# Performance work log

Measured on AMD Instinct MI355X. Metric: run time of the kernel, lower is better.

The kernel has to match this reference:

```python
import jax, jax.numpy as jnp
import numpy as np
import math

B, S, D, H = 2, 2048, 2048, 16
HD = D // H  # head_dim = 128


def _rope_tables(seq_len, head_dim, theta=10000.0):
    inv = 1.0 / (theta ** (np.arange(0, head_dim, 2, dtype=np.float32) / head_dim))
    t = np.arange(seq_len, dtype=np.float32)
    freqs = np.outer(t, inv)  # [S, HD/2]
    return jnp.asarray(np.cos(freqs)), jnp.asarray(np.sin(freqs))


def setup_inputs() -> dict:
    key = jax.random.key(0)
    ks = jax.random.split(key, 6)
    std = 1.0 / math.sqrt(D)
    x = jax.random.normal(ks[0], (B, S, D), dtype=jnp.float32)
    wq_w = jax.random.normal(ks[1], (D, D), dtype=jnp.float32) * std
    wk_w = jax.random.normal(ks[2], (D, D), dtype=jnp.float32) * std
    wv_w = jax.random.normal(ks[3], (D, D), dtype=jnp.float32) * std
    wo_w = jax.random.normal(ks[4], (D, D), dtype=jnp.float32) * std
    zb = jnp.zeros((D,), dtype=jnp.float32)
    fc, fs = _rope_tables(S, HD)
    return {"x": x, "wq_w": wq_w, "wq_b": zb, "wk_w": wk_w, "wk_b": zb,
            "wv_w": wv_w, "wv_b": zb, "wo_w": wo_w, "wo_b": zb,
            "freqs_cos": fc, "freqs_sin": fs}


def _apply_rope(q, k, cos, sin):
    # q, k: [B, S, H, HD]; cos/sin: [S, HD/2] -> broadcast [1, S, 1, HD/2]
    cos = cos[None, :, None, :]
    sin = sin[None, :, None, :]

    def rot(t):
        tr, ti = t[..., 0::2], t[..., 1::2]
        orr = tr * cos - ti * sin
        oi = tr * sin + ti * cos
        return jnp.stack([orr, oi], axis=-1).reshape(t.shape)

    return rot(q), rot(k)


def reference(x, wq_w, wq_b, wk_w, wk_b, wv_w, wv_b, wo_w, wo_b, freqs_cos, freqs_sin):
    b, s, d = x.shape
    q = (x @ wq_w.T + wq_b).reshape(b, s, H, HD)
    k = (x @ wk_w.T + wk_b).reshape(b, s, H, HD)
    v = (x @ wv_w.T + wv_b).reshape(b, s, H, HD)
    q, k = _apply_rope(q, k, freqs_cos[:s], freqs_sin[:s])
    q = q.transpose(0, 2, 1, 3)  # [B,H,S,HD]
    k = k.transpose(0, 2, 1, 3)
    v = v.transpose(0, 2, 1, 3)
    scale = math.sqrt(HD)
    scores = jnp.einsum('bhqd,bhkd->bhqk', q, k) / scale
    causal = jnp.tril(jnp.ones((s, s), dtype=bool))
    scores = jnp.where(causal[None, None], scores, jnp.float32(-jnp.inf))
    attn = jax.nn.softmax(scores, axis=-1)
    out = jnp.einsum('bhqk,bhkd->bhqd', attn, v)
    out = out.transpose(0, 2, 1, 3).reshape(b, s, d)
    out = out @ wo_w.T + wo_b
    return out, k, v
```

## Files before the change

kernel.cpp:

```cpp
#include <hip/hip_runtime.h>

#define B_  2
#define S_  2048
#define D_  2048
#define H_  16
#define HD_ 128

#define QSCALE 0.1275174319003887f

typedef __attribute__((ext_vector_type(4))) float  f32x4;
typedef __attribute__((ext_vector_type(8))) short  short8;
typedef __attribute__((ext_vector_type(8))) __bf16 bf16x8;
typedef __attribute__((ext_vector_type(4))) float  floatv4;
typedef __attribute__((ext_vector_type(4))) unsigned short ushortv4;

__device__ inline unsigned short f2bf(float f) {
  unsigned int u = __builtin_bit_cast(unsigned int, f);
  u += 0x7fffu + ((u >> 16) & 1u);
  return (unsigned short)(u >> 16);
}

__device__ inline void gld16(void* lds, const void* g) {
  __builtin_amdgcn_global_load_lds(
      (const __attribute__((address_space(1))) unsigned int*)g,
      (__attribute__((address_space(3))) unsigned int*)lds, 16, 0, 0);
}

__device__ inline bf16x8 lds_frag_b(const void* p) {
  return __builtin_bit_cast(bf16x8, *(const short8*)p);
}

__global__ void cvt_all(const float* __restrict__ x,
                        const float* __restrict__ w0, const float* __restrict__ w1,
                        const float* __restrict__ w2, const float* __restrict__ w3,
                        unsigned short* __restrict__ xb,
                        unsigned short* __restrict__ wb0, unsigned short* __restrict__ wb1,
                        unsigned short* __restrict__ wb2, unsigned short* __restrict__ wb3) {
  int i = blockIdx.x * 256 + threadIdx.x;
  const float* s; unsigned short* d; int off;
  if (i < 2097152) { s = x; d = xb; off = i; }
  else {
    int j = i - 2097152;
    int r = j >> 20; off = j & 1048575;
    s = (r == 0) ? w0 : (r == 1) ? w1 : (r == 2) ? w2 : w3;
    d = (r == 0) ? wb0 : (r == 1) ? wb1 : (r == 2) ? wb2 : wb3;
  }
  floatv4 v = ((const floatv4*)s)[off];
  ushortv4 o;
  o.x = f2bf(v.x); o.y = f2bf(v.y); o.z = f2bf(v.z); o.w = f2bf(v.w);
  ((ushortv4*)d)[off] = o;
}

template<int MI0, int NJ0>
__device__ inline void quad_mm(f32x4 (&acc)[4][4], const bf16x8 (&af)[2][2], const bf16x8 (&bf)[2][2]) {
#pragma unroll
  for (int mi = 0; mi < 2; ++mi)
#pragma unroll
    for (int nj = 0; nj < 2; ++nj)
#pragma unroll
      for (int ks = 0; ks < 2; ++ks)
        acc[MI0 + mi][NJ0 + nj] =
            __builtin_amdgcn_mfma_f32_16x16x32_bf16(af[mi][ks], bf[nj][ks], acc[MI0 + mi][NJ0 + nj], 0, 0, 0);
}

__device__ inline void stage(char* ldsbuf, int chunk, const char* gtile, int w, long thrOff) {
  gld16(ldsbuf + chunk * 8192 + w * 1024, gtile + (long)chunk * 64 * 4096 + thrOff);
}

#define RDF(dst, buf, baserow)                                                          \
  do {                                                                                  \
    int _r0 = (baserow);                                                                \
    _Pragma("unroll") for (int _ii = 0; _ii < 2; ++_ii) {                               \
      int _row = _r0 + _ii * 16;                                                        \
      _Pragma("unroll") for (int _ks = 0; _ks < 2; ++_ks)                               \
          dst[_ii][_ks] = lds_frag_b((buf) + _row * 128 + ((_ks * 64 + quad * 16) ^ xsw)); \
    }                                                                                   \
  } while (0)

#define GBAR() __builtin_amdgcn_s_barrier()
#define LGK0()                                                 \
  do {                                                         \
    asm volatile("s_waitcnt lgkmcnt(0)" ::: "memory");         \
    __builtin_amdgcn_sched_barrier(0);                         \
  } while (0)

template<int MODE>
__global__ __launch_bounds__(512, 1)
void gemm8p(const unsigned short* __restrict__ A,
            const unsigned short* __restrict__ W,
            const float* __restrict__ b0, const float* __restrict__ b1, const float* __restrict__ b2,
            float* __restrict__ CQ,
            float* __restrict__ CK,
            float* __restrict__ v_out,
            int nbx) {
  __shared__ __attribute__((aligned(16))) char smem[98304];
  char* As0 = smem;
  char* As1 = smem + 32768;
  char* Bs0 = smem + 65536;
  char* Bs1 = smem + 81920;

  const int t = threadIdx.x, w = t >> 6, lane = t & 63;
  const int quad = lane >> 4, l16 = lane & 15;
  const int wm = (w >> 1) * 64, wn = (w & 1) * 64;
  const int xsw = (l16 & 7) << 4;

  const int nwg = gridDim.x, q8 = nwg >> 3;
  const int wg = ((int)blockIdx.x & 7) * q8 + ((int)blockIdx.x >> 3);
  const int by = wg / nbx, bx = wg % nbx;
  const int m0 = by * 256, n0 = bx * 128;

  const char* Agl = (const char*)A + (size_t)m0 * 4096;
  const char* Wgl = (const char*)W + (size_t)n0 * 4096;
  const int sr = t >> 3;
  const long thrOff = (long)sr * 4096 + (((t & 7) * 16) ^ ((sr & 7) << 4));

#pragma unroll
  for (int c = 0; c < 4; ++c) stage(As0, c, Agl, w, thrOff);
#pragma unroll
  for (int c = 0; c < 2; ++c) stage(Bs0, c, Wgl, w, thrOff);
#pragma unroll
  for (int c = 0; c < 4; ++c) stage(As1, c, Agl + 128, w, thrOff);
#pragma unroll
  for (int c = 0; c < 2; ++c) stage(Bs1, c, Wgl + 128, w, thrOff);
  asm volatile("s_waitcnt vmcnt(6)" ::: "memory");
  GBAR();

  f32x4 acc[4][4] = {};

  for (int it = 0; it < 16; ++it) {
    int s0 = 2 * it + 2; if (s0 >= 32) s0 -= 2;
    int s1 = 2 * it + 3; if (s1 >= 32) s1 -= 2;
    const char* As0g = Agl + (long)s0 * 128;
    const char* Bs0g = Wgl + (long)s0 * 128;
    const char* As1g = Agl + (long)s1 * 128;
    const char* Bs1g = Wgl + (long)s1 * 128;
    bf16x8 a01[2][2], a23[2][2], b01[2][2], b23[2][2];

    RDF(a01, As0, wm + l16);
    RDF(b01, Bs0, wn + l16);
    GBAR(); LGK0();
    __builtin_amdgcn_s_setprio(1); quad_mm<0, 0>(acc, a01, b01); __builtin_amdgcn_s_setprio(0);
    GBAR();
    RDF(a23, As0, wm + 32 + l16);
    GBAR(); LGK0();
    __builtin_amdgcn_s_setprio(1); quad_mm<2, 0>(acc, a23, b01); __builtin_amdgcn_s_setprio(0);
    GBAR();
    RDF(b23, Bs0, wn + 32 + l16);
    stage(As0, 0, As0g, w, thrOff); stage(As0, 1, As0g, w, thrOff);
    GBAR(); LGK0();
    __builtin_amdgcn_s_setprio(1); quad_mm<0, 2>(acc, a01, b23); __builtin_amdgcn_s_setprio(0);
    GBAR();
    stage(As0, 2, As0g, w, thrOff); stage(As0, 3, As0g, w, thrOff);
    GBAR(); LGK0();
    __builtin_amdgcn_s_setprio(1); quad_mm<2, 2>(acc, a23, b23); __builtin_amdgcn_s_setprio(0);
    asm volatile("s_waitcnt vmcnt(4)" ::: "memory");
    GBAR();
    RDF(a01, As1, wm + l16);
    RDF(b01, Bs1, wn + l16);
    stage(Bs0, 0, Bs0g, w, thrOff); stage(Bs0, 1, Bs0g, w, thrOff);
    GBAR(); LGK0();
    __builtin_amdgcn_s_setprio(1); quad_mm<0, 0>(acc, a01, b01); __builtin_amdgcn_s_setprio(0);
    GBAR();
    RDF(a23, As1, wm + 32 + l16);
    GBAR(); LGK0();
    __builtin_amdgcn_s_setprio(1); quad_mm<2, 0>(acc, a23, b01); __builtin_amdgcn_s_setprio(0);
    GBAR();
    RDF(b23, Bs1, wn + 32 + l16);
    stage(As1, 0, As1g, w, thrOff); stage(As1, 1, As1g, w, thrOff);
    GBAR(); LGK0();
    __builtin_amdgcn_s_setprio(1); quad_mm<0, 2>(acc, a01, b23); __builtin_amdgcn_s_setprio(0);
    GBAR();
    stage(As1, 2, As1g, w, thrOff); stage(As1, 3, As1g, w, thrOff);
    stage(Bs1, 0, Bs1g, w, thrOff); stage(Bs1, 1, Bs1g, w, thrOff);
    GBAR(); LGK0();
    __builtin_amdgcn_s_setprio(1); quad_mm<2, 2>(acc, a23, b23); __builtin_amdgcn_s_setprio(0);
    asm volatile("s_waitcnt vmcnt(6)" ::: "memory");
    GBAR();
  }

  asm volatile("s_waitcnt vmcnt(0)" ::: "memory");

  if constexpr (MODE == 1) {
#pragma unroll
    for (int nj = 0; nj < 4; ++nj) {
      int col = n0 + wn + nj * 16 + l16;
      int sel = col >> 11;
      int cc  = col & 2047;
      const float* bp = (sel == 0) ? b0 : (sel == 1) ? b1 : b2;
      float bv = bp[cc];
#pragma unroll
      for (int mi = 0; mi < 4; ++mi)
#pragma unroll
        for (int r = 0; r < 4; ++r) {
          int row = m0 + wm + mi * 16 + quad * 4 + r;
          float v = acc[mi][nj][r] + bv;
          if (sel == 0) {
            CQ[(size_t)row * 2048 + cc] = v;
          } else if (sel == 1) {
            CK[(size_t)row * 2048 + cc] = v;
          } else {
            int s = row & 2047, bb = row >> 11;
            int hh = cc >> 7, d = cc & 127;
            v_out[((size_t)(bb * H_ + hh) * S_ + s) * HD_ + d] = v;
          }
        }
    }
  } else {
#pragma unroll
    for (int nj = 0; nj < 4; ++nj) {
      int col = n0 + wn + nj * 16 + l16;
      float bv = b0[col];
#pragma unroll
      for (int mi = 0; mi < 4; ++mi)
#pragma unroll
        for (int r = 0; r < 4; ++r) {
          int row = m0 + wm + mi * 16 + quad * 4 + r;
          CQ[(size_t)row * 2048 + col] = acc[mi][nj][r] + bv;
        }
    }
  }
}

__global__ void rope_vtrans(const float* __restrict__ Qbuf,
                            const float* __restrict__ Kbuf,
                            const float* __restrict__ fc,
                            const float* __restrict__ fs,
                            unsigned short* __restrict__ Qa,
                            unsigned short* __restrict__ Ka,
                            float* __restrict__ k_out,
                            const float* __restrict__ Vsrc,
                            unsigned short* __restrict__ Vt) {
  __shared__ float tile[64][33];
  int bx = blockIdx.x;
  int t = threadIdx.x;
  if (bx < 16384) {
    int idx = bx * 256 + t;
    int i = idx & 63;
    int h = (idx >> 6) & (H_ - 1);
    int s = (idx >> 10) & (S_ - 1);
    int b = idx >> 21;
    size_t src = ((size_t)(b * S_ + s)) * D_ + h * HD_ + 2 * i;
    float2 q = *(const float2*)(Qbuf + src);
    float2 k = *(const float2*)(Kbuf + src);
    float c = fc[s * 64 + i], sn = fs[s * 64 + i];
    float qor = q.x * c - q.y * sn, qoi = q.x * sn + q.y * c;
    float kor = k.x * c - k.y * sn, koi = k.x * sn + k.y * c;
    size_t dst = ((size_t)((b * H_ + h) * S_ + s)) * HD_ + 2 * i;
    *(unsigned int*)(Qa + dst) = (unsigned int)f2bf(qor * QSCALE) | ((unsigned int)f2bf(qoi * QSCALE) << 16);
    *(unsigned int*)(Ka + dst) = (unsigned int)f2bf(kor) | ((unsigned int)f2bf(koi) << 16);
    *(float2*)(k_out + dst) = make_float2(kor, koi);
  } else {
    int v = bx - 16384;
    int s0 = (v & 31) * 64, d0 = ((v >> 5) & 3) * 32, bh = v >> 7;
#pragma unroll
    for (int rr = 0; rr < 8; ++rr) {
      int sl = rr * 8 + (t >> 5), dl = t & 31;
      tile[sl][dl] = Vsrc[((size_t)(bh * S_ + s0 + sl)) * HD_ + d0 + dl];
    }
    __syncthreads();
#pragma unroll
    for (int rr = 0; rr < 8; ++rr) {
      int dl = rr * 4 + (t >> 6), sl = t & 63;
      Vt[((size_t)(bh * HD_ + d0 + dl)) * S_ + s0 + sl] = f2bf(tile[sl][dl]);
    }
  }
}

__global__ __launch_bounds__(256, 2)
void attn_kernel(const unsigned short* __restrict__ Qa,
                 const unsigned short* __restrict__ Ka,
                 const unsigned short* __restrict__ Vt,
                 unsigned short* __restrict__ Oa) {
  __shared__ __attribute__((aligned(16))) unsigned short Ks[2][64 * 128];
  __shared__ __attribute__((aligned(16))) unsigned short Vs[128 * 64];
  __shared__ __attribute__((aligned(16))) unsigned short Ps[4][16 * 64];
  const int t = threadIdx.x, w = t >> 6, lane = t & 63;
  const int quad = lane >> 4, l16 = lane & 15;
  const int bid = blockIdx.x;
  const int bh = (bid & 7) + 8 * (bid >> 7);
  const int p  = (bid >> 3) & 15;
  const int b = bh >> 4, h = bh & 15;
  const unsigned short* Qp = Qa + (size_t)bh * S_ * HD_;
  const unsigned short* Kp = Ka + (size_t)bh * S_ * HD_;
  const unsigned short* Vp = Vt + (size_t)bh * HD_ * S_;
  const float NEGINF = -__builtin_inff();

  for (int part = 0; part < 2; ++part) {
    const int qs = part ? (31 - p) : p;
    const int q0 = qs * 64;
    const int ntmax = qs;

    __syncthreads();

#pragma unroll
    for (int j = 0; j < 4; ++j) {
      int o = (t + 256 * j) * 16;
      int row = o >> 8, cb = (o & 255) ^ ((row & 7) << 4);
      gld16((char*)Ks[0] + w * 1024 + j * 4096, (const char*)(Kp + (size_t)row * HD_) + cb);
    }
    bf16x8 qf[4];
#pragma unroll
    for (int kk = 0; kk < 4; ++kk)
      qf[kk] = *(const bf16x8*)(Qp + (size_t)(q0 + w * 16 + l16) * HD_ + kk * 32 + quad * 8);

    float m_i[4], l_i[4];
#pragma unroll
    for (int r = 0; r < 4; ++r) { m_i[r] = NEGINF; l_i[r] = 0.f; }
    f32x4 oacc[8] = {};
    int c = 0;

    for (int nt = 0; nt <= ntmax; ++nt) {
      __syncthreads();

#pragma unroll
      for (int j = 0; j < 4; ++j) {
        int o = (t + 256 * j) * 16;
        int vrow = o >> 7, vcb = (o & 127) ^ ((vrow & 7) << 4);
        gld16((char*)Vs + w * 1024 + j * 4096,
              (const char*)(Vp + (size_t)vrow * S_ + nt * 64) + vcb);
      }

      f32x4 sacc[4] = {};
      const char* Kc = (const char*)Ks[c];
      __builtin_amdgcn_s_setprio(1);
#pragma unroll
      for (int j = 0; j < 4; ++j) {
        int krow = j * 16 + l16;
        const char* kbase = Kc + krow * 256;
        int ksw = (krow & 7) << 4;
#pragma unroll
        for (int kk = 0; kk < 4; ++kk) {
          bf16x8 kf = lds_frag_b(kbase + ((kk * 64 + quad * 16) ^ ksw));
          sacc[j] = __builtin_amdgcn_mfma_f32_16x16x32_bf16(qf[kk], kf, sacc[j], 0, 0, 0);
        }
      }
      __builtin_amdgcn_s_setprio(0);

      const bool dotail = (nt == ntmax);
      float rowmax[4], alpha[4], rowsum[4];
#pragma unroll
      for (int r = 0; r < 4; ++r) rowmax[r] = NEGINF;
#pragma unroll
      for (int j = 0; j < 4; ++j) {
        int scol = nt * 64 + j * 16 + l16;
#pragma unroll
        for (int r = 0; r < 4; ++r) {
          float v = sacc[j][r];
          if (dotail && scol > q0 + w * 16 + quad * 4 + r) v = NEGINF;
          sacc[j][r] = v;
          rowmax[r] = fmaxf(rowmax[r], v);
        }
      }
#pragma unroll
      for (int off = 1; off < 16; off <<= 1)
#pragma unroll
        for (int r = 0; r < 4; ++r)
          rowmax[r] = fmaxf(rowmax[r], __shfl_xor(rowmax[r], off));
#pragma unroll
      for (int r = 0; r < 4; ++r) {
        float mnew = fmaxf(m_i[r], rowmax[r]);
        alpha[r] = __builtin_amdgcn_exp2f(m_i[r] - mnew);
        m_i[r] = mnew;
        rowsum[r] = 0.f;
      }
#pragma unroll
      for (int j = 0; j < 4; ++j)
#pragma unroll
        for (int r = 0; r < 4; ++r) {
          float e = __builtin_amdgcn_exp2f(sacc[j][r] - m_i[r]);
          sacc[j][r] = e;
          rowsum[r] += e;
        }
#pragma unroll
      for (int off = 1; off < 16; off <<= 1)
#pragma unroll
        for (int r = 0; r < 4; ++r)
          rowsum[r] += __shfl_xor(rowsum[r], off);
#pragma unroll
      for (int r = 0; r < 4; ++r) l_i[r] = l_i[r] * alpha[r] + rowsum[r];
#pragma unroll
      for (int f = 0; f < 8; ++f)
#pragma unroll
        for (int r = 0; r < 4; ++r) oacc[f][r] *= alpha[r];

      __syncthreads();

      if (nt < ntmax) {
#pragma unroll
        for (int j = 0; j < 4; ++j) {
          int o = (t + 256 * j) * 16;
          int row = o >> 8, cb = (o & 255) ^ ((row & 7) << 4);
          gld16((char*)Ks[c ^ 1] + w * 1024 + j * 4096,
                (const char*)(Kp + (size_t)((nt + 1) * 64 + row) * HD_) + cb);
        }
      }

      char* Pw = (char*)&Ps[w][0];
#pragma unroll
      for (int j = 0; j < 4; ++j)
#pragma unroll
        for (int r = 0; r < 4; ++r) {
          int prow = quad * 4 + r;
          *(unsigned short*)(Pw + prow * 128 + ((2 * (j * 16 + l16)) ^ ((prow & 7) << 4))) = f2bf(sacc[j][r]);
        }
      asm volatile("s_waitcnt lgkmcnt(0)" ::: "memory");

      const char* Vb = (const char*)Vs;
      int psw = (l16 & 7) << 4;
      __builtin_amdgcn_s_setprio(1);
#pragma unroll
      for (int s2 = 0; s2 < 2; ++s2) {
        bf16x8 pf = lds_frag_b(Pw + l16 * 128 + ((s2 * 64 + quad * 16) ^ psw));
#pragma unroll
        for (int f = 0; f < 8; ++f) {
          int vrow = f * 16 + l16;
          bf16x8 vf = lds_frag_b(Vb + vrow * 128 + ((s2 * 64 + quad * 16) ^ ((vrow & 7) << 4)));
          oacc[f] = __builtin_amdgcn_mfma_f32_16x16x32_bf16(pf, vf, oacc[f], 0, 0, 0);
        }
      }
      __builtin_amdgcn_s_setprio(0);
      c ^= 1;
    }

    float invl[4];
#pragma unroll
    for (int r = 0; r < 4; ++r) invl[r] = 1.f / l_i[r];
#pragma unroll
    for (int f = 0; f < 8; ++f)
#pragma unroll
      for (int r = 0; r < 4; ++r) {
        int srow = q0 + w * 16 + quad * 4 + r;
        int d = f * 16 + l16;
        Oa[((size_t)(b * S_ + srow)) * D_ + h * HD_ + d] = f2bf(oacc[f][r] * invl[r]);
      }
  }
}

extern "C" void kernel_launch(void* const* d_in, const int* in_sizes, int n_in,
                              void* d_out, int out_size, void* d_ws, size_t ws_size,
                              hipStream_t stream) {
  const float* x    = (const float*)d_in[0];
  const float* wq_w = (const float*)d_in[1];
  const float* wq_b = (const float*)d_in[2];
  const float* wk_w = (const float*)d_in[3];
  const float* wk_b = (const float*)d_in[4];
  const float* wv_w = (const float*)d_in[5];
  const float* wv_b = (const float*)d_in[6];
  const float* wo_w = (const float*)d_in[7];
  const float* wo_b = (const float*)d_in[8];
  const float* fc   = (const float*)d_in[9];
  const float* fs   = (const float*)d_in[10];

  float* out = (float*)d_out;
  const size_t BSD = (size_t)B_ * S_ * D_;
  float* k_out = out + BSD;
  float* v_out = out + 2 * BSD;

  char* ws = (char*)d_ws;
  unsigned short* xb   = (unsigned short*)(ws);
  unsigned short* wqb  = (unsigned short*)(ws + 16777216);
  unsigned short* wkb  = (unsigned short*)(ws + 25165824);
  unsigned short* wvb  = (unsigned short*)(ws + 33554432);
  unsigned short* wob  = (unsigned short*)(ws + 41943040);
  float*          Kbuf = (float*)(ws + 50331648);
  unsigned short* Qat  = (unsigned short*)(ws + 83886080);
  unsigned short* Kat  = (unsigned short*)(ws + 100663296);
  unsigned short* Vt   = (unsigned short*)(ws + 117440512);
  unsigned short* Ab   = (unsigned short*)(ws + 134217728);

  float* Qbuf = out;

  cvt_all<<<24576, 256, 0, stream>>>(x, wq_w, wk_w, wv_w, wo_w, xb, wqb, wkb, wvb, wob);

  gemm8p<1><<<dim3(768), 512, 0, stream>>>(xb, wqb, wq_b, wk_b, wv_b,
                                           Qbuf, Kbuf, v_out, 48);

  rope_vtrans<<<20480, 256, 0, stream>>>(Qbuf, Kbuf, fc, fs, Qat, Kat, k_out, v_out, Vt);

  attn_kernel<<<512, 256, 0, stream>>>(Qat, Kat, Vt, Ab);

  gemm8p<0><<<dim3(256), 512, 0, stream>>>(Ab, wob, wo_b, nullptr, nullptr,
                                           out, nullptr, nullptr, 16);
}
```

Measured before the change: 455.8 us.

## Use 256x256 tiles for fused QKV GEMM and drop setprio in attention

Adds a dedicated QKV projection kernel with 256x256 output tiles (8 waves each computing 128x64), replacing the 256x128-tile templated GEMM, and uses 128KB LDS for double-buffered A/B tiles. Larger tiles halve the block count and raise arithmetic intensity per byte loaded from global memory and LDS. The cost is more accumulator registers and fewer blocks (384) to spread across CUs, plus a new staging and wait schedule. It also removes s_setprio hints around the MFMA loops in the attention kernel.

```diff
diff --git a/kernel.cpp b/kernel.cpp
--- a/kernel.cpp
+++ b/kernel.cpp
@@ -51,32 +51,6 @@
   ((ushortv4*)d)[off] = o;
 }
 
-template<int MI0, int NJ0>
-__device__ inline void quad_mm(f32x4 (&acc)[4][4], const bf16x8 (&af)[2][2], const bf16x8 (&bf)[2][2]) {
-#pragma unroll
-  for (int mi = 0; mi < 2; ++mi)
-#pragma unroll
-    for (int nj = 0; nj < 2; ++nj)
-#pragma unroll
-      for (int ks = 0; ks < 2; ++ks)
-        acc[MI0 + mi][NJ0 + nj] =
-            __builtin_amdgcn_mfma_f32_16x16x32_bf16(af[mi][ks], bf[nj][ks], acc[MI0 + mi][NJ0 + nj], 0, 0, 0);
-}
-
-__device__ inline void stage(char* ldsbuf, int chunk, const char* gtile, int w, long thrOff) {
-  gld16(ldsbuf + chunk * 8192 + w * 1024, gtile + (long)chunk * 64 * 4096 + thrOff);
-}
-
-#define RDF(dst, buf, baserow)                                                          \
-  do {                                                                                  \
-    int _r0 = (baserow);                                                                \
-    _Pragma("unroll") for (int _ii = 0; _ii < 2; ++_ii) {                               \
-      int _row = _r0 + _ii * 16;                                                        \
-      _Pragma("unroll") for (int _ks = 0; _ks < 2; ++_ks)                               \
-          dst[_ii][_ks] = lds_frag_b((buf) + _row * 128 + ((_ks * 64 + quad * 16) ^ xsw)); \
-    }                                                                                   \
-  } while (0)
-
 #define GBAR() __builtin_amdgcn_s_barrier()
 #define LGK0()                                                 \
   do {                                                         \
@@ -84,14 +58,47 @@
     __builtin_amdgcn_sched_barrier(0);                         \
   } while (0)
 
-template<int MODE>
+__device__ inline void stage(char* ldsbuf, int chunk, const char* gtile, int w, long thrOff) {
+  gld16(ldsbuf + chunk * 8192 + w * 1024, gtile + (long)chunk * 64 * 4096 + thrOff);
+}
+
+#define RDF2(dst, buf, baserow)                                                          \
+  do {                                                                                   \
+    int _r0 = (baserow);                                                                 \
+    _Pragma("unroll") for (int _ii = 0; _ii < 2; ++_ii) {                                \
+      int _row = _r0 + _ii * 16;                                                         \
+      _Pragma("unroll") for (int _ks = 0; _ks < 2; ++_ks)                                \
+          dst[_ii][_ks] = lds_frag_b((buf) + _row * 128 + ((_ks * 64 + quad * 16) ^ xsw)); \
+    }                                                                                    \
+  } while (0)
+
+#define RDF4(dst, buf, baserow)                                                          \
+  do {                                                                                   \
+    int _r0 = (baserow);                                                                 \
+    _Pragma("unroll") for (int _ii = 0; _ii < 4; ++_ii) {                                \
+      int _row = _r0 + _ii * 16;                                                         \
+      _Pragma("unroll") for (int _ks = 0; _ks < 2; ++_ks)                                \
+          dst[_ii][_ks] = lds_frag_b((buf) + _row * 128 + ((_ks * 64 + quad * 16) ^ xsw)); \
+    }                                                                                    \
+  } while (0)
+
+template<int MI0, int NJ0>
+__device__ inline void quad_mm(f32x4 (&acc)[4][4], const bf16x8 (&af)[2][2], const bf16x8 (&bf)[2][2]) {
+#pragma unroll
+  for (int mi = 0; mi < 2; ++mi)
+#pragma unroll
+    for (int nj = 0; nj < 2; ++nj)
+#pragma unroll
+      for (int ks = 0; ks < 2; ++ks)
+        acc[MI0 + mi][NJ0 + nj] =
+            __builtin_amdgcn_mfma_f32_16x16x32_bf16(af[mi][ks], bf[nj][ks], acc[MI0 + mi][NJ0 + nj], 0, 0, 0);
+}
+
 __global__ __launch_bounds__(512, 1)
 void gemm8p(const unsigned short* __restrict__ A,
             const unsigned short* __restrict__ W,
-            const float* __restrict__ b0, const float* __restrict__ b1, const float* __restrict__ b2,
-            float* __restrict__ CQ,
-            float* __restrict__ CK,
-            float* __restrict__ v_out,
+            const float* __restrict__ b0,
+            float* __restrict__ C0,
             int nbx) {
   __shared__ __attribute__((aligned(16))) char smem[98304];
   char* As0 = smem;
@@ -136,16 +143,16 @@
     const char* Bs1g = Wgl + (long)s1 * 128;
     bf16x8 a01[2][2], a23[2][2], b01[2][2], b23[2][2];
 
-    RDF(a01, As0, wm + l16);
-    RDF(b01, Bs0, wn + l16);
+    RDF2(a01, As0, wm + l16);
+    RDF2(b01, Bs0, wn + l16);
     GBAR(); LGK0();
     __builtin_amdgcn_s_setprio(1); quad_mm<0, 0>(acc, a01, b01); __builtin_amdgcn_s_setprio(0);
     GBAR();
-    RDF(a23, As0, wm + 32 + l16);
+    RDF2(a23, As0, wm + 32 + l16);
     GBAR(); LGK0();
     __builtin_amdgcn_s_setprio(1); quad_mm<2, 0>(acc, a23, b01); __builtin_amdgcn_s_setprio(0);
     GBAR();
-    RDF(b23, Bs0, wn + 32 + l16);
+    RDF2(b23, Bs0, wn + 32 + l16);
     stage(As0, 0, As0g, w, thrOff); stage(As0, 1, As0g, w, thrOff);
     GBAR(); LGK0();
     __builtin_amdgcn_s_setprio(1); quad_mm<0, 2>(acc, a01, b23); __builtin_amdgcn_s_setprio(0);
@@ -155,17 +162,17 @@
     __builtin_amdgcn_s_setprio(1); quad_mm<2, 2>(acc, a23, b23); __builtin_amdgcn_s_setprio(0);
     asm volatile("s_waitcnt vmcnt(4)" ::: "memory");
     GBAR();
-    RDF(a01, As1, wm + l16);
-    RDF(b01, Bs1, wn + l16);
+    RDF2(a01, As1, wm + l16);
+    RDF2(b01, Bs1, wn + l16);
     stage(Bs0, 0, Bs0g, w, thrOff); stage(Bs0, 1, Bs0g, w, thrOff);
     GBAR(); LGK0();
     __builtin_amdgcn_s_setprio(1); quad_mm<0, 0>(acc, a01, b01); __builtin_amdgcn_s_setprio(0);
     GBAR();
-    RDF(a23, As1, wm + 32 + l16);
+    RDF2(a23, As1, wm + 32 + l16);
     GBAR(); LGK0();
     __builtin_amdgcn_s_setprio(1); quad_mm<2, 0>(acc, a23, b01); __builtin_amdgcn_s_setprio(0);
     GBAR();
-    RDF(b23, Bs1, wn + 32 + l16);
+    RDF2(b23, Bs1, wn + 32 + l16);
     stage(As1, 0, As1g, w, thrOff); stage(As1, 1, As1g, w, thrOff);
     GBAR(); LGK0();
     __builtin_amdgcn_s_setprio(1); quad_mm<0, 2>(acc, a01, b23); __builtin_amdgcn_s_setprio(0);
@@ -180,44 +187,148 @@
 
   asm volatile("s_waitcnt vmcnt(0)" ::: "memory");
 
-  if constexpr (MODE == 1) {
-#pragma unroll
-    for (int nj = 0; nj < 4; ++nj) {
-      int col = n0 + wn + nj * 16 + l16;
-      int sel = col >> 11;
-      int cc  = col & 2047;
-      const float* bp = (sel == 0) ? b0 : (sel == 1) ? b1 : b2;
-      float bv = bp[cc];
-#pragma unroll
-      for (int mi = 0; mi < 4; ++mi)
-#pragma unroll
-        for (int r = 0; r < 4; ++r) {
-          int row = m0 + wm + mi * 16 + quad * 4 + r;
-          float v = acc[mi][nj][r] + bv;
-          if (sel == 0) {
-            CQ[(size_t)row * 2048 + cc] = v;
-          } else if (sel == 1) {
-            CK[(size_t)row * 2048 + cc] = v;
-          } else {
-            int s = row & 2047, bb = row >> 11;
-            int hh = cc >> 7, d = cc & 127;
-            v_out[((size_t)(bb * H_ + hh) * S_ + s) * HD_ + d] = v;
-          }
-        }
-    }
-  } else {
-#pragma unroll
-    for (int nj = 0; nj < 4; ++nj) {
-      int col = n0 + wn + nj * 16 + l16;
-      float bv = b0[col];
-#pragma unroll
-      for (int mi = 0; mi < 4; ++mi)
-#pragma unroll
-        for (int r = 0; r < 4; ++r) {
-          int row = m0 + wm + mi * 16 + quad * 4 + r;
-          CQ[(size_t)row * 2048 + col] = acc[mi][nj][r] + bv;
-        }
-    }
+#pragma unroll
+  for (int nj = 0; nj < 4; ++nj) {
+    int col = n0 + wn + nj * 16 + l16;
+    float bv = b0[col];
+#pragma unroll
+    for (int mi = 0; mi < 4; ++mi)
+#pragma unroll
+      for (int r = 0; r < 4; ++r) {
+        int row = m0 + wm + mi * 16 + quad * 4 + r;
+        C0[(size_t)row * 2048 + col] = acc[mi][nj][r] + bv;
+      }
+  }
+}
+
+template<int MH, int NH>
+__device__ inline void mm16(f32x4 (&acc)[8][4], const bf16x8 (&af)[4][2], const bf16x8 (&bf)[2][2]) {
+#pragma unroll
+  for (int mi = 0; mi < 4; ++mi)
+#pragma unroll
+    for (int nj = 0; nj < 2; ++nj)
+#pragma unroll
+      for (int ks = 0; ks < 2; ++ks)
+        acc[MH * 4 + mi][NH * 2 + nj] =
+            __builtin_amdgcn_mfma_f32_16x16x32_bf16(af[mi][ks], bf[nj][ks], acc[MH * 4 + mi][NH * 2 + nj], 0, 0, 0);
+}
+
+__global__ __launch_bounds__(512, 1)
+void gemm256_qkv(const unsigned short* __restrict__ A,
+                 const unsigned short* __restrict__ W,
+                 const float* __restrict__ b0, const float* __restrict__ b1, const float* __restrict__ b2,
+                 float* __restrict__ CQ, float* __restrict__ CK, float* __restrict__ v_out) {
+  __shared__ __attribute__((aligned(16))) char smem[131072];
+  char* As0 = smem;
+  char* As1 = smem + 32768;
+  char* Bs0 = smem + 65536;
+  char* Bs1 = smem + 98304;
+
+  const int t = threadIdx.x, w = t >> 6, lane = t & 63;
+  const int quad = lane >> 4, l16 = lane & 15;
+  const int wm = (w >> 2) * 128, wn = (w & 3) * 64;
+  const int xsw = (l16 & 7) << 4;
+
+  const int wg = ((int)blockIdx.x & 7) * 48 + ((int)blockIdx.x >> 3);
+  const int by = wg / 24, bx = wg % 24;
+  const int m0 = by * 256, n0 = bx * 256;
+
+  const char* Agl = (const char*)A + (size_t)m0 * 4096;
+  const char* Wgl = (const char*)W + (size_t)n0 * 4096;
+  const int sr = t >> 3;
+  const long thrOff = (long)sr * 4096 + (((t & 7) * 16) ^ ((sr & 7) << 4));
+
+#pragma unroll
+  for (int c = 0; c < 4; ++c) stage(As0, c, Agl, w, thrOff);
+#pragma unroll
+  for (int c = 0; c < 4; ++c) stage(Bs0, c, Wgl, w, thrOff);
+#pragma unroll
+  for (int c = 0; c < 4; ++c) stage(As1, c, Agl + 128, w, thrOff);
+#pragma unroll
+  for (int c = 0; c < 4; ++c) stage(Bs1, c, Wgl + 128, w, thrOff);
+  asm volatile("s_waitcnt vmcnt(8)" ::: "memory");
+  GBAR();
+
+  f32x4 acc[8][4] = {};
+
+  for (int it = 0; it < 16; ++it) {
+    int s0 = 2 * it + 2; if (s0 >= 32) s0 -= 2;
+    int s1 = 2 * it + 3; if (s1 >= 32) s1 -= 2;
+    const char* As0g = Agl + (long)s0 * 128;
+    const char* Bs0g = Wgl + (long)s0 * 128;
+    const char* As1g = Agl + (long)s1 * 128;
+    const char* Bs1g = Wgl + (long)s1 * 128;
+    bf16x8 a[4][2], bl[2][2], bh[2][2];
+
+    RDF4(a, As0, wm + l16);
+    RDF2(bl, Bs0, wn + l16);
+    GBAR(); LGK0();
+    __builtin_amdgcn_s_setprio(1); mm16<0, 0>(acc, a, bl); __builtin_amdgcn_s_setprio(0);
+    GBAR();
+    RDF2(bh, Bs0, wn + 32 + l16);
+    stage(As0, 0, As0g, w, thrOff); stage(As0, 2, As0g, w, thrOff);
+    GBAR(); LGK0();
+    __builtin_amdgcn_s_setprio(1); mm16<0, 1>(acc, a, bh); __builtin_amdgcn_s_setprio(0);
+    GBAR();
+    RDF4(a, As0, wm + 64 + l16);
+    stage(Bs0, 0, Bs0g, w, thrOff); stage(Bs0, 1, Bs0g, w, thrOff);
+    stage(Bs0, 2, Bs0g, w, thrOff); stage(Bs0, 3, Bs0g, w, thrOff);
+    GBAR(); LGK0();
+    __builtin_amdgcn_s_setprio(1); mm16<1, 1>(acc, a, bh); __builtin_amdgcn_s_setprio(0);
+    GBAR();
+    stage(As0, 1, As0g, w, thrOff); stage(As0, 3, As0g, w, thrOff);
+    GBAR(); LGK0();
+    __builtin_amdgcn_s_setprio(1); mm16<1, 0>(acc, a, bl); __builtin_amdgcn_s_setprio(0);
+    asm volatile("s_waitcnt vmcnt(8)" ::: "memory");
+    GBAR();
+    RDF4(a, As1, wm + l16);
+    RDF2(bl, Bs1, wn + l16);
+    GBAR(); LGK0();
+    __builtin_amdgcn_s_setprio(1); mm16<0, 0>(acc, a, bl); __builtin_amdgcn_s_setprio(0);
+    GBAR();
+    RDF2(bh, Bs1, wn + 32 + l16);
+    stage(As1, 0, As1g, w, thrOff); stage(As1, 2, As1g, w, thrOff);
+    GBAR(); LGK0();
+    __builtin_amdgcn_s_setprio(1); mm16<0, 1>(acc, a, bh); __builtin_amdgcn_s_setprio(0);
+    GBAR();
+    RDF4(a, As1, wm + 64 + l16);
+    stage(Bs1, 0, Bs1g, w, thrOff); stage(Bs1, 1, Bs1g, w, thrOff);
+    stage(Bs1, 2, Bs1g, w, thrOff); stage(Bs1, 3, Bs1g, w, thrOff);
+    GBAR(); LGK0();
+    __builtin_amdgcn_s_setprio(1); mm16<1, 1>(acc, a, bh); __builtin_amdgcn_s_setprio(0);
+    GBAR();
+    stage(As1, 1, As1g, w, thrOff); stage(As1, 3, As1g, w, thrOff);
+    GBAR(); LGK0();
+    __builtin_amdgcn_s_setprio(1); mm16<1, 0>(acc, a, bl); __builtin_amdgcn_s_setprio(0);
+    asm volatile("s_waitcnt vmcnt(8)" ::: "memory");
+    GBAR();
+  }
+
+  asm volatile("s_waitcnt vmcnt(0)" ::: "memory");
+
+  const int sel = (n0 >> 11);
+#pragma unroll
+  for (int nf = 0; nf < 4; ++nf) {
+    int col = n0 + wn + nf * 16 + l16;
+    int cc  = col & 2047;
+    const float* bp = (sel == 0) ? b0 : (sel == 1) ? b1 : b2;
+    float bv = bp[cc];
+#pragma unroll
+    for (int mf = 0; mf < 8; ++mf)
+#pragma unroll
+      for (int r = 0; r < 4; ++r) {
+        int row = m0 + wm + mf * 16 + quad * 4 + r;
+        float v = acc[mf][nf][r] + bv;
+        if (sel == 0) {
+          CQ[(size_t)row * 2048 + cc] = v;
+        } else if (sel == 1) {
+          CK[(size_t)row * 2048 + cc] = v;
+        } else {
+          int s = row & 2047, bb = row >> 11;
+          int hh = cc >> 7, d = cc & 127;
+          v_out[((size_t)(bb * H_ + hh) * S_ + s) * HD_ + d] = v;
+        }
+      }
   }
 }
 
@@ -322,7 +433,6 @@
 
       f32x4 sacc[4] = {};
       const char* Kc = (const char*)Ks[c];
-      __builtin_amdgcn_s_setprio(1);
 #pragma unroll
       for (int j = 0; j < 4; ++j) {
         int krow = j * 16 + l16;
@@ -334,7 +444,6 @@
           sacc[j] = __builtin_amdgcn_mfma_f32_16x16x32_bf16(qf[kk], kf, sacc[j], 0, 0, 0);
         }
       }
-      __builtin_amdgcn_s_setprio(0);
 
       const bool dotail = (nt == ntmax);
       float rowmax[4], alpha[4], rowsum[4];
@@ -407,7 +516,6 @@
 
       const char* Vb = (const char*)Vs;
       int psw = (l16 & 7) << 4;
-      __builtin_amdgcn_s_setprio(1);
 #pragma unroll
       for (int s2 = 0; s2 < 2; ++s2) {
         bf16x8 pf = lds_frag_b(Pw + l16 * 128 + ((s2 * 64 + quad * 16) ^ psw));
@@ -418,7 +526,6 @@
           oacc[f] = __builtin_amdgcn_mfma_f32_16x16x32_bf16(pf, vf, oacc[f], 0, 0, 0);
         }
       }
-      __builtin_amdgcn_s_setprio(0);
       c ^= 1;
     }
 
@@ -472,13 +579,12 @@
 
   cvt_all<<<24576, 256, 0, stream>>>(x, wq_w, wk_w, wv_w, wo_w, xb, wqb, wkb, wvb, wob);
 
-  gemm8p<1><<<dim3(768), 512, 0, stream>>>(xb, wqb, wq_b, wk_b, wv_b,
-                                           Qbuf, Kbuf, v_out, 48);
+  gemm256_qkv<<<dim3(384), 512, 0, stream>>>(xb, wqb, wq_b, wk_b, wv_b,
+                                             Qbuf, Kbuf, v_out);
 
   rope_vtrans<<<20480, 256, 0, stream>>>(Qbuf, Kbuf, fc, fs, Qat, Kat, k_out, v_out, Vt);
 
   attn_kernel<<<512, 256, 0, stream>>>(Qat, Kat, Vt, Ab);
 
-  gemm8p<0><<<dim3(256), 512, 0, stream>>>(Ab, wob, wo_b, nullptr, nullptr,
-                                           out, nullptr, nullptr, 16);
-}
+  gemm8p<<<dim3(256), 512, 0, stream>>>(Ab, wob, wo_b, out, 16);
+}
```

Measured after the change: 453.9 us. About the same (-0.4%).
